# Kernel tuning notes

Measured on AMD Instinct MI355X. Metric: run time of the kernel, lower is better.

The kernel has to match this reference:

```python
import jax, jax.numpy as jnp
import numpy as np

ALPHA = 0.2  # LeakyReLU negative slope
V_NODES = 7  # fixed by the module (self.B, self.A are 7x7)


def setup_inputs() -> dict:
    key = jax.random.key(0)
    k1, k2, k3 = jax.random.split(key, 3)
    N, C, T, V = 64, 256, 256, V_NODES
    F = 256  # out_features
    h = jax.random.normal(k1, (N, C, T, V), dtype=jnp.float32)
    # xavier_uniform with gain=1.414 ~ U(-b, b), b = gain*sqrt(6/(fan_in+fan_out))
    bW = 1.414 * np.sqrt(6.0 / (T + F))
    W = jax.random.uniform(k2, (T, F), dtype=jnp.float32, minval=-bW, maxval=bW)
    ba = 1.414 * np.sqrt(6.0 / (2 * F + 1))
    a = jax.random.uniform(k3, (2 * F, 1), dtype=jnp.float32, minval=-ba, maxval=ba)
    B = jnp.zeros((V, V), dtype=jnp.float32) + 1e-6
    return {"h": h, "W": W, "a": a, "B": B}


def reference(h, W, a, B):
    # h: (N, C, T, V) -> (N, V, C, T)
    h = jnp.transpose(h, (0, 3, 1, 2))
    Wh = jnp.matmul(h, W)                       # (N, V, C, F)
    F = Wh.shape[-1]
    a1 = a[:F, 0]                               # (F,)
    a2 = a[F:, 0]                               # (F,)
    # e[n,i,j,c] = a1.Wh[n,i,c,:] + a2.Wh[n,j,c,:]  (avoids (N,V,V,C,2F) materialization)
    s1 = jnp.einsum('nicf,f->nic', Wh, a1)      # (N, V, C)
    s2 = jnp.einsum('njcf,f->njc', Wh, a2)      # (N, V, C)
    e = s1[:, :, None, :] + s2[:, None, :, :]   # (N, V, V, C)
    e = jnp.where(e > 0, e, ALPHA * e)          # LeakyReLU
    att = jax.nn.softmax(e, axis=-1)            # softmax over channel dim C
    # normalized adjacency: min-max then symmetric degree normalization
    V_ = B.shape[0]
    adj = B + jnp.eye(V_, dtype=B.dtype)
    adj = (adj - jnp.min(adj)) / (jnp.max(adj) - jnp.min(adj))
    d_inv_sqrt = 1.0 / jnp.sqrt(jnp.sum(adj, axis=1))
    adj_norm = adj * d_inv_sqrt[:, None] * d_inv_sqrt[None, :]
    # diag_embed(att) matmul loop == channel-wise weighted sum over j
    h_agg = jnp.einsum('njcf,nijc->nicf', Wh, att)        # (N, V, C, F)
    out = jnp.einsum('nicf,iv->ncfv', h_agg, adj_norm)    # (N, C, F, V)
    return jax.nn.elu(out)
```

## Files before the change

kernel.cpp:

```cpp
#include <hip/hip_runtime.h>
#include <hip/hip_bf16.h>

#define LRELU_ALPHA 0.2f

typedef __attribute__((ext_vector_type(8))) short short8;
typedef __attribute__((ext_vector_type(4))) float f32x4;

__device__ __forceinline__ float bf2f(unsigned short u) {
  union { unsigned int i; float f; } x;
  x.i = ((unsigned int)u) << 16;
  return x.f;
}

__global__ __launch_bounds__(256) void k0_wt(const float* __restrict__ W,
                                             __hip_bfloat16* __restrict__ Wt) {
  int t = blockIdx.x, f = threadIdx.x;
  Wt[f * 256 + t] = __float2bfloat16(W[t * 256 + f]);
}

__global__ __launch_bounds__(64) void k0_wa(const float* __restrict__ W,
                                            const float* __restrict__ a,
                                            float* __restrict__ Wa) {
  int t = blockIdx.x, lane = threadIdx.x;
  float4 wv = *reinterpret_cast<const float4*>(W + t * 256 + lane * 4);
  float4 a1 = *reinterpret_cast<const float4*>(a + lane * 4);
  float4 a2 = *reinterpret_cast<const float4*>(a + 256 + lane * 4);
  float p1 = wv.x * a1.x + wv.y * a1.y + wv.z * a1.z + wv.w * a1.w;
  float p2 = wv.x * a2.x + wv.y * a2.y + wv.z * a2.z + wv.w * a2.w;
  #pragma unroll
  for (int off = 32; off; off >>= 1) {
    p1 += __shfl_down(p1, off);
    p2 += __shfl_down(p2, off);
  }
  if (lane == 0) { Wa[t] = p1; Wa[256 + t] = p2; }
}

__global__ __launch_bounds__(64) void k0_adj(const float* __restrict__ B,
                                             float* __restrict__ adjn) {
  int t = threadIdx.x;
  float v = 0.f;
  if (t < 49) v = B[t] + (((t / 7) == (t % 7)) ? 1.f : 0.f);
  float mn = (t < 49) ? v : 1e30f;
  float mx = (t < 49) ? v : -1e30f;
  #pragma unroll
  for (int off = 32; off; off >>= 1) {
    mn = fminf(mn, __shfl_xor(mn, off));
    mx = fmaxf(mx, __shfl_xor(mx, off));
  }
  float scaled = (v - mn) / (mx - mn);
  __shared__ float adj[49];
  __shared__ float dis[7];
  if (t < 49) adj[t] = scaled;
  __syncthreads();
  if (t < 7) {
    float s = 0.f;
    #pragma unroll
    for (int j = 0; j < 7; ++j) s += adj[t * 7 + j];
    dis[t] = 1.0f / sqrtf(s);
  }
  __syncthreads();
  if (t < 49) adjn[t] = adj[t] * dis[t / 7] * dis[t % 7];
}

__global__ __launch_bounds__(256) void k1_gemm(const float* __restrict__ h,
                                               const __hip_bfloat16* __restrict__ Wt,
                                               const float* __restrict__ Wa,
                                               __hip_bfloat16* __restrict__ Wh,
                                               float* __restrict__ s1g,
                                               float* __restrict__ s2g) {
  __shared__ __hip_bfloat16 As[56][264];
  __shared__ short BsS[256 * 40];
  const int blk = blockIdx.x;
  const int n = blk >> 5, cb = blk & 31;
  const int tid = threadIdx.x;

  const short* WtS = reinterpret_cast<const short*>(Wt);

  int bf[4], bkc[4];
  #pragma unroll
  for (int it = 0; it < 4; ++it) {
    int idx16 = tid + it * 256;
    bf[it] = idx16 >> 2;
    bkc[it] = idx16 & 3;
  }

  const float4* src =
      reinterpret_cast<const float4*>(h + (size_t)(n * 256 + cb * 8) * 1792);
  float4 vals[14];
  #pragma unroll
  for (int it = 0; it < 14; ++it) vals[it] = src[tid + it * 256];

  short8 breg[4];
  #pragma unroll
  for (int it = 0; it < 4; ++it)
    breg[it] = *reinterpret_cast<const short8*>(WtS + bf[it] * 256 + bkc[it] * 8);

  #pragma unroll
  for (int it = 0; it < 14; ++it) {
    int base = (tid + it * 256) * 4;
    const float* vp = reinterpret_cast<const float*>(&vals[it]);
    #pragma unroll
    for (int q = 0; q < 4; ++q) {
      int idx = base + q;
      int c = idx / 1792;
      int r = idx - c * 1792;
      int t = r / 7;
      int v = r - t * 7;
      As[c * 7 + v][t] = __float2bfloat16(vp[q]);
    }
  }
  #pragma unroll
  for (int it = 0; it < 4; ++it)
    *reinterpret_cast<short8*>(BsS + bf[it] * 40 + bkc[it] * 8) = breg[it];
  __syncthreads();

  const int lane = tid & 63, wave = tid >> 6;
  const int lr = lane & 15, lk = lane >> 4;
  const int f_base = wave * 64;

  f32x4 acc[4][4];
  #pragma unroll
  for (int mt = 0; mt < 4; ++mt)
    #pragma unroll
    for (int ft = 0; ft < 4; ++ft) acc[mt][ft] = (f32x4){0.f, 0.f, 0.f, 0.f};

  const short* AsS = reinterpret_cast<const short*>(&As[0][0]);

  int rowm[4];
  #pragma unroll
  for (int mt = 0; mt < 4; ++mt) {
    int m = mt * 16 + lr;
    rowm[mt] = (m < 56) ? m : 55;
  }

  #pragma unroll
  for (int kb = 0; kb < 8; ++kb) {
    short8 bnext[4];
    if (kb < 7) {
      #pragma unroll
      for (int it = 0; it < 4; ++it)
        bnext[it] = *reinterpret_cast<const short8*>(
            WtS + bf[it] * 256 + (kb + 1) * 32 + bkc[it] * 8);
    }
    short8 bfrag[4];
    #pragma unroll
    for (int ft = 0; ft < 4; ++ft)
      bfrag[ft] = *reinterpret_cast<const short8*>(
          BsS + (f_base + ft * 16 + lr) * 40 + lk * 8);
    #pragma unroll
    for (int mt = 0; mt < 4; ++mt) {
      short8 afrag = *reinterpret_cast<const short8*>(
          AsS + rowm[mt] * 264 + kb * 32 + lk * 8);
      #pragma unroll
      for (int ft = 0; ft < 4; ++ft)
        acc[mt][ft] = __builtin_amdgcn_mfma_f32_16x16x32_bf16(afrag, bfrag[ft],
                                                              acc[mt][ft], 0, 0, 0);
    }
    __syncthreads();
    if (kb < 7) {
      #pragma unroll
      for (int it = 0; it < 4; ++it)
        *reinterpret_cast<short8*>(BsS + bf[it] * 40 + bkc[it] * 8) = bnext[it];
      __syncthreads();
    }
  }

  #pragma unroll
  for (int mt = 0; mt < 4; ++mt) {
    #pragma unroll
    for (int j = 0; j < 4; ++j) {
      int m = mt * 16 + lk * 4 + j;
      if (m < 56) {
        int cl = m / 7;
        int v = m - cl * 7;
        __hip_bfloat16* dst =
            Wh + (size_t)((n * 256 + cb * 8 + cl) * 7 + v) * 256 + f_base + lr;
        #pragma unroll
        for (int ft = 0; ft < 4; ++ft)
          dst[ft * 16] = __float2bfloat16(acc[mt][ft][j]);
      }
    }
  }

  const int gid = tid >> 4;
  const int fl = tid & 15;
  float wa1[16], wa2[16];
  #pragma unroll
  for (int q = 0; q < 16; ++q) {
    wa1[q] = Wa[fl * 16 + q];
    wa2[q] = Wa[256 + fl * 16 + q];
  }
  #pragma unroll
  for (int k = 0; k < 4; ++k) {
    int m = k * 16 + gid;
    if (m < 56) {
      short8 r0 = *reinterpret_cast<const short8*>(AsS + m * 264 + fl * 16);
      short8 r1 = *reinterpret_cast<const short8*>(AsS + m * 264 + fl * 16 + 8);
      float p1 = 0.f, p2 = 0.f;
      #pragma unroll
      for (int q = 0; q < 8; ++q) {
        float x = bf2f((unsigned short)r0[q]);
        p1 += x * wa1[q];
        p2 += x * wa2[q];
        float y = bf2f((unsigned short)r1[q]);
        p1 += y * wa1[8 + q];
        p2 += y * wa2[8 + q];
      }
      #pragma unroll
      for (int off = 1; off <= 8; off <<= 1) {
        p1 += __shfl_xor(p1, off);
        p2 += __shfl_xor(p2, off);
      }
      if (fl == 0) {
        int cl = m / 7, v = m - cl * 7;
        int c = cb * 8 + cl;
        s1g[(n * 7 + v) * 256 + c] = p1;
        s2g[(n * 7 + v) * 256 + c] = p2;
      }
    }
  }
}

__global__ __launch_bounds__(256) void k2_soft(const float* __restrict__ s1g,
                                               const float* __restrict__ s2g,
                                               float* __restrict__ att) {
  __shared__ float s1L[1792], s2L[1792];
  const int n = blockIdx.x, tid = threadIdx.x;
  for (int idx = tid; idx < 1792; idx += 256) {
    s1L[idx] = s1g[n * 1792 + idx];
    s2L[idx] = s2g[n * 1792 + idx];
  }
  __syncthreads();
  const int lane = tid & 63, wave = tid >> 6;
  for (int p = wave; p < 49; p += 4) {
    int i = p / 7, j = p - i * 7;
    float ex[4];
    float mx = -1e30f;
    #pragma unroll
    for (int q = 0; q < 4; ++q) {
      int c = lane + q * 64;
      float e = s1L[i * 256 + c] + s2L[j * 256 + c];
      e = (e > 0.f) ? e : LRELU_ALPHA * e;
      ex[q] = e;
      mx = fmaxf(mx, e);
    }
    #pragma unroll
    for (int off = 32; off; off >>= 1) mx = fmaxf(mx, __shfl_xor(mx, off));
    float sm = 0.f;
    #pragma unroll
    for (int q = 0; q < 4; ++q) {
      ex[q] = __expf(ex[q] - mx);
      sm += ex[q];
    }
    #pragma unroll
    for (int off = 32; off; off >>= 1) sm += __shfl_xor(sm, off);
    float inv = 1.0f / sm;
    #pragma unroll
    for (int q = 0; q < 4; ++q) {
      int c = lane + q * 64;
      att[((size_t)n * 256 + c) * 49 + p] = ex[q] * inv;
    }
  }
}

__global__ __launch_bounds__(256) void k3_out(const __hip_bfloat16* __restrict__ Wh,
                                              const float* __restrict__ att,
                                              const float* __restrict__ adjn,
                                              float* __restrict__ out) {
  __shared__ float attL[49], adjL[49], M[49];
  __shared__ float outL[1792];
  const int blk = blockIdx.x;
  const int n = blk >> 8, c = blk & 255;
  const int tid = threadIdx.x;
  if (tid < 49) {
    attL[tid] = att[((size_t)n * 256 + c) * 49 + tid];
    adjL[tid] = adjn[tid];
  }
  __syncthreads();
  if (tid < 49) {
    int j = tid / 7, v = tid - (tid / 7) * 7;
    float s = 0.f;
    #pragma unroll
    for (int i = 0; i < 7; ++i) s += attL[i * 7 + j] * adjL[i * 7 + v];
    M[tid] = s;
  }
  __syncthreads();
  const unsigned short* WhS = reinterpret_cast<const unsigned short*>(Wh) +
                              ((size_t)n * 256 + c) * 1792 + tid;
  float wh[7];
  #pragma unroll
  for (int j = 0; j < 7; ++j) wh[j] = bf2f(WhS[j * 256]);
  #pragma unroll
  for (int v = 0; v < 7; ++v) {
    float o = 0.f;
    #pragma unroll
    for (int j = 0; j < 7; ++j) o += wh[j] * M[j * 7 + v];
    o = (o > 0.f) ? o : (__expf(o) - 1.f);
    outL[tid * 7 + v] = o;
  }
  __syncthreads();
  float* dst = out + (size_t)(n * 256 + c) * 1792;
  for (int idx = tid; idx < 1792; idx += 256) dst[idx] = outL[idx];
}

extern "C" void kernel_launch(void* const* d_in, const int* in_sizes, int n_in,
                              void* d_out, int out_size, void* d_ws, size_t ws_size,
                              hipStream_t stream) {
  const float* h = (const float*)d_in[0];
  const float* W = (const float*)d_in[1];
  const float* a = (const float*)d_in[2];
  const float* B = (const float*)d_in[3];
  float* out = (float*)d_out;
  char* ws = (char*)d_ws;

  __hip_bfloat16* Wt = (__hip_bfloat16*)(ws + 0);
  float* adjn = (float*)(ws + 131072);
  float* Wa   = (float*)(ws + 131328);
  float* s1g  = (float*)(ws + 133376);
  float* s2g  = (float*)(ws + 592128);
  float* att  = (float*)(ws + 1050880);
  __hip_bfloat16* Wh = (__hip_bfloat16*)(ws + 4262144);

  k0_wt<<<256, 256, 0, stream>>>(W, Wt);
  k0_wa<<<256, 64, 0, stream>>>(W, a, Wa);
  k0_adj<<<1, 64, 0, stream>>>(B, adjn);
  k1_gemm<<<2048, 256, 0, stream>>>(h, Wt, Wa, Wh, s1g, s2g);
  k2_soft<<<64, 256, 0, stream>>>(s1g, s2g, att);
  k3_out<<<16384, 256, 0, stream>>>(Wh, att, adjn, out);
}
```

Measured before the change: 111.1 us.

## Split score kernel from GEMM, read B from global, stage Wh stores through LDS

The fused GEMM+score kernel is split into two kernels: a separate k1s computes s1/s2 directly from fp32 h, and k1g does the GEMM only. k1g drops the LDS double-buffering of Wt and reads B fragments directly from global/L2, which removes the per-k-step barriers. It also loads h with a per-thread contiguous pattern to transpose into LDS, and writes Wh through LDS so the global stores are coalesced 16-byte rows. The cost is a second full read of h (about 117 MB) in k1s, plus an extra kernel launch.

```diff
diff --git a/kernel.cpp b/kernel.cpp
--- a/kernel.cpp
+++ b/kernel.cpp
@@ -4,12 +4,19 @@
 #define LRELU_ALPHA 0.2f
 
 typedef __attribute__((ext_vector_type(8))) short short8;
+typedef __attribute__((ext_vector_type(4))) short short4v;
 typedef __attribute__((ext_vector_type(4))) float f32x4;
 
 __device__ __forceinline__ float bf2f(unsigned short u) {
   union { unsigned int i; float f; } x;
   x.i = ((unsigned int)u) << 16;
   return x.f;
+}
+__device__ __forceinline__ short f2bf(float f) {
+  __hip_bfloat16 b = __float2bfloat16(f);
+  union { __hip_bfloat16 b; short s; } u;
+  u.b = b;
+  return u.s;
 }
 
 __global__ __launch_bounds__(256) void k0_wt(const float* __restrict__ W,
@@ -62,56 +69,86 @@
   if (t < 49) adjn[t] = adj[t] * dis[t / 7] * dis[t % 7];
 }
 
-__global__ __launch_bounds__(256) void k1_gemm(const float* __restrict__ h,
-                                               const __hip_bfloat16* __restrict__ Wt,
-                                               const float* __restrict__ Wa,
-                                               __hip_bfloat16* __restrict__ Wh,
-                                               float* __restrict__ s1g,
-                                               float* __restrict__ s2g) {
-  __shared__ __hip_bfloat16 As[56][264];
-  __shared__ short BsS[256 * 40];
+__global__ __launch_bounds__(256) void k1s(const float* __restrict__ h,
+                                           const float* __restrict__ Wa,
+                                           float* __restrict__ s1g,
+                                           float* __restrict__ s2g) {
+  const int blk = blockIdx.x;
+  const int n = blk >> 4, cs = blk & 15;
+  const int tid = threadIdx.x;
+  const int lane = tid & 63, wave = tid >> 6;
+  float wa1[4], wa2[4];
+  #pragma unroll
+  for (int q = 0; q < 4; ++q) {
+    wa1[q] = Wa[lane * 4 + q];
+    wa2[q] = Wa[256 + lane * 4 + q];
+  }
+  #pragma unroll
+  for (int ci = 0; ci < 4; ++ci) {
+    int c = cs * 16 + wave * 4 + ci;
+    const float4* src =
+        reinterpret_cast<const float4*>(h + (size_t)(n * 256 + c) * 1792 + lane * 28);
+    float4 x[7];
+    #pragma unroll
+    for (int i = 0; i < 7; ++i) x[i] = src[i];
+    const float* xf = reinterpret_cast<const float*>(x);
+    float p1[7], p2[7];
+    #pragma unroll
+    for (int v = 0; v < 7; ++v) { p1[v] = 0.f; p2[v] = 0.f; }
+    #pragma unroll
+    for (int dt = 0; dt < 4; ++dt)
+      #pragma unroll
+      for (int v = 0; v < 7; ++v) {
+        float val = xf[dt * 7 + v];
+        p1[v] += val * wa1[dt];
+        p2[v] += val * wa2[dt];
+      }
+    #pragma unroll
+    for (int v = 0; v < 7; ++v) {
+      #pragma unroll
+      for (int off = 32; off; off >>= 1) {
+        p1[v] += __shfl_xor(p1[v], off);
+        p2[v] += __shfl_xor(p2[v], off);
+      }
+    }
+    if (lane == 0) {
+      #pragma unroll
+      for (int v = 0; v < 7; ++v) {
+        s1g[(n * 7 + v) * 256 + c] = p1[v];
+        s2g[(n * 7 + v) * 256 + c] = p2[v];
+      }
+    }
+  }
+}
+
+__global__ __launch_bounds__(256) void k1g(const float* __restrict__ h,
+                                           const __hip_bfloat16* __restrict__ Wt,
+                                           __hip_bfloat16* __restrict__ Wh) {
+  __shared__ short As[56 * 264];
   const int blk = blockIdx.x;
   const int n = blk >> 5, cb = blk & 31;
   const int tid = threadIdx.x;
 
-  const short* WtS = reinterpret_cast<const short*>(Wt);
-
-  int bf[4], bkc[4];
-  #pragma unroll
-  for (int it = 0; it < 4; ++it) {
-    int idx16 = tid + it * 256;
-    bf[it] = idx16 >> 2;
-    bkc[it] = idx16 & 3;
-  }
-
-  const float4* src =
-      reinterpret_cast<const float4*>(h + (size_t)(n * 256 + cb * 8) * 1792);
-  float4 vals[14];
-  #pragma unroll
-  for (int it = 0; it < 14; ++it) vals[it] = src[tid + it * 256];
-
-  short8 breg[4];
-  #pragma unroll
-  for (int it = 0; it < 4; ++it)
-    breg[it] = *reinterpret_cast<const short8*>(WtS + bf[it] * 256 + bkc[it] * 8);
-
-  #pragma unroll
-  for (int it = 0; it < 14; ++it) {
-    int base = (tid + it * 256) * 4;
-    const float* vp = reinterpret_cast<const float*>(&vals[it]);
-    #pragma unroll
-    for (int q = 0; q < 4; ++q) {
-      int idx = base + q;
-      int c = idx / 1792;
-      int r = idx - c * 1792;
-      int t = r / 7;
-      int v = r - t * 7;
-      As[c * 7 + v][t] = __float2bfloat16(vp[q]);
-    }
-  }
-  #pragma unroll
-  for (int it = 0; it < 4; ++it)
-    *reinterpret_cast<short8*>(BsS + bf[it] * 40 + bkc[it] * 8) = breg[it];
+  {
+    const int c8 = tid >> 5;
+    const int t0 = (tid & 31) * 8;
+    const float* src = h + (size_t)((n * 256 + cb * 8 + c8)) * 1792 + t0 * 7;
+    #pragma unroll
+    for (int th = 0; th < 2; ++th) {
+      float4 x[7];
+      #pragma unroll
+      for (int i = 0; i < 7; ++i)
+        x[i] = reinterpret_cast<const float4*>(src + th * 28)[i];
+      const float* xf = reinterpret_cast<const float*>(x);
+      #pragma unroll
+      for (int v = 0; v < 7; ++v) {
+        short4v row;
+        #pragma unroll
+        for (int dt = 0; dt < 4; ++dt) row[dt] = f2bf(xf[dt * 7 + v]);
+        *reinterpret_cast<short4v*>(As + (c8 * 7 + v) * 264 + t0 + th * 4) = row;
+      }
+    }
+  }
   __syncthreads();
 
   const int lane = tid & 63, wave = tid >> 6;
@@ -124,7 +161,7 @@
     #pragma unroll
     for (int ft = 0; ft < 4; ++ft) acc[mt][ft] = (f32x4){0.f, 0.f, 0.f, 0.f};
 
-  const short* AsS = reinterpret_cast<const short*>(&As[0][0]);
+  const short* WtS = reinterpret_cast<const short*>(Wt);
 
   int rowm[4];
   #pragma unroll
@@ -135,35 +172,23 @@
 
   #pragma unroll
   for (int kb = 0; kb < 8; ++kb) {
-    short8 bnext[4];
-    if (kb < 7) {
-      #pragma unroll
-      for (int it = 0; it < 4; ++it)
-        bnext[it] = *reinterpret_cast<const short8*>(
-            WtS + bf[it] * 256 + (kb + 1) * 32 + bkc[it] * 8);
-    }
     short8 bfrag[4];
     #pragma unroll
     for (int ft = 0; ft < 4; ++ft)
       bfrag[ft] = *reinterpret_cast<const short8*>(
-          BsS + (f_base + ft * 16 + lr) * 40 + lk * 8);
+          WtS + (f_base + ft * 16 + lr) * 256 + kb * 32 + lk * 8);
     #pragma unroll
     for (int mt = 0; mt < 4; ++mt) {
       short8 afrag = *reinterpret_cast<const short8*>(
-          AsS + rowm[mt] * 264 + kb * 32 + lk * 8);
+          As + rowm[mt] * 264 + kb * 32 + lk * 8);
       #pragma unroll
       for (int ft = 0; ft < 4; ++ft)
         acc[mt][ft] = __builtin_amdgcn_mfma_f32_16x16x32_bf16(afrag, bfrag[ft],
                                                               acc[mt][ft], 0, 0, 0);
     }
-    __syncthreads();
-    if (kb < 7) {
-      #pragma unroll
-      for (int it = 0; it < 4; ++it)
-        *reinterpret_cast<short8*>(BsS + bf[it] * 40 + bkc[it] * 8) = bnext[it];
-      __syncthreads();
-    }
-  }
+  }
+
+  __syncthreads();
 
   #pragma unroll
   for (int mt = 0; mt < 4; ++mt) {
@@ -171,53 +196,21 @@
     for (int j = 0; j < 4; ++j) {
       int m = mt * 16 + lk * 4 + j;
       if (m < 56) {
-        int cl = m / 7;
-        int v = m - cl * 7;
-        __hip_bfloat16* dst =
-            Wh + (size_t)((n * 256 + cb * 8 + cl) * 7 + v) * 256 + f_base + lr;
         #pragma unroll
         for (int ft = 0; ft < 4; ++ft)
-          dst[ft * 16] = __float2bfloat16(acc[mt][ft][j]);
-      }
-    }
-  }
-
-  const int gid = tid >> 4;
-  const int fl = tid & 15;
-  float wa1[16], wa2[16];
-  #pragma unroll
-  for (int q = 0; q < 16; ++q) {
-    wa1[q] = Wa[fl * 16 + q];
-    wa2[q] = Wa[256 + fl * 16 + q];
-  }
-  #pragma unroll
-  for (int k = 0; k < 4; ++k) {
-    int m = k * 16 + gid;
-    if (m < 56) {
-      short8 r0 = *reinterpret_cast<const short8*>(AsS + m * 264 + fl * 16);
-      short8 r1 = *reinterpret_cast<const short8*>(AsS + m * 264 + fl * 16 + 8);
-      float p1 = 0.f, p2 = 0.f;
-      #pragma unroll
-      for (int q = 0; q < 8; ++q) {
-        float x = bf2f((unsigned short)r0[q]);
-        p1 += x * wa1[q];
-        p2 += x * wa2[q];
-        float y = bf2f((unsigned short)r1[q]);
-        p1 += y * wa1[8 + q];
-        p2 += y * wa2[8 + q];
-      }
-      #pragma unroll
-      for (int off = 1; off <= 8; off <<= 1) {
-        p1 += __shfl_xor(p1, off);
-        p2 += __shfl_xor(p2, off);
-      }
-      if (fl == 0) {
-        int cl = m / 7, v = m - cl * 7;
-        int c = cb * 8 + cl;
-        s1g[(n * 7 + v) * 256 + c] = p1;
-        s2g[(n * 7 + v) * 256 + c] = p2;
-      }
-    }
+          As[m * 264 + f_base + ft * 16 + lr] = f2bf(acc[mt][ft][j]);
+      }
+    }
+  }
+  __syncthreads();
+
+  short* dst = reinterpret_cast<short*>(Wh) + (size_t)(n * 256 + cb * 8) * 1792;
+  #pragma unroll
+  for (int pass = 0; pass < 7; ++pass) {
+    int r = pass * 8 + (tid >> 5);
+    int col = tid & 31;
+    short8 vrow = *reinterpret_cast<const short8*>(As + r * 264 + col * 8);
+    *reinterpret_cast<short8*>(dst + r * 256 + col * 8) = vrow;
   }
 }
 
@@ -324,7 +317,8 @@
   k0_wt<<<256, 256, 0, stream>>>(W, Wt);
   k0_wa<<<256, 64, 0, stream>>>(W, a, Wa);
   k0_adj<<<1, 64, 0, stream>>>(B, adjn);
-  k1_gemm<<<2048, 256, 0, stream>>>(h, Wt, Wa, Wh, s1g, s2g);
+  k1s<<<1024, 256, 0, stream>>>(h, Wa, s1g, s2g);
+  k1g<<<2048, 256, 0, stream>>>(h, Wt, Wh);
   k2_soft<<<64, 256, 0, stream>>>(s1g, s2g, att);
   k3_out<<<16384, 256, 0, stream>>>(Wh, att, adjn, out);
 }
```

After: 129.7 us. +16.8%, slower.
